# Performance work log

Hardware: AMD Instinct MI355X
Metric: run time of the kernel (lower is better)

## Reference

```python
import jax, jax.numpy as jnp
import numpy as np

K = 9          # kernel_size
PAD = K // 2   # 'same' padding, stride 1
SIGMA = 1.0
EPS = 1e-5     # BatchNorm eps

def _windows(a):
    # a: (B, C, L) -> (B, C, K, L); zero-padded sliding windows (== F.unfold semantics)
    L = a.shape[-1]
    ap = jnp.pad(a, ((0, 0), (0, 0), (PAD, PAD)))
    return jnp.stack([ap[:, :, k:k + L] for k in range(K)], axis=2)

def setup_inputs() -> dict:
    key = jax.random.key(0)
    ks = jax.random.split(key, 4)
    B, Cin, Cout, L = 8, 256, 256, 16384
    x = jax.random.normal(ks[0], (B, Cin, L), jnp.float32)
    coords = jax.random.uniform(ks[1], (B, 3, L), jnp.float32)
    conv_w = jax.random.normal(ks[2], (Cout, Cin, K), jnp.float32) * np.float32(1.0 / np.sqrt(Cin * K))
    conv_b = jnp.zeros((Cout,), jnp.float32)
    gamma = jnp.ones((Cout,), jnp.float32)
    beta = jnp.zeros((Cout,), jnp.float32)
    return {"x": x, "coords": coords, "conv_w": conv_w, "conv_b": conv_b, "gamma": gamma, "beta": beta}

def reference(x, coords, conv_w, conv_b, gamma, beta):
    # --- WeightedConv1D: Gaussian coordinate weights on each unfolded window element ---
    cw = _windows(coords)                                      # (B, 3, K, L)
    d2 = jnp.sum((cw - coords[:, :, None, :]) ** 2, axis=1)    # (B, K, L) squared dist to window center
    w = jnp.exp(-d2 / (2.0 * SIGMA ** 2))                      # (B, K, L) Gaussian weights
    xw = _windows(x) * w[:, None, :, :]                        # (B, Cin, K, L) weighted windows
    y = jnp.einsum('bckl,ock->bol', xw, conv_w) + conv_b[None, :, None]  # (B, Cout, L)
    # --- BatchNorm1d (training-mode batch statistics, biased variance) + ReLU ---
    mu = jnp.mean(y, axis=(0, 2), keepdims=True)
    var = jnp.var(y, axis=(0, 2), keepdims=True)
    yhat = (y - mu) * jax.lax.rsqrt(var + EPS)
    out = jax.nn.relu(yhat * gamma[None, :, None] + beta[None, :, None])
    # Dropout with drop=0.0 is the identity.
    return out
```

## Files before the change

### kernel.cpp

```cpp
#include <hip/hip_runtime.h>
#include <hip/hip_bf16.h>


typedef float        f32x4  __attribute__((ext_vector_type(4)));
typedef short        bf16x8 __attribute__((ext_vector_type(8)));
typedef unsigned int u32x4  __attribute__((ext_vector_type(4)));

#define LLEN 16384

__device__ __forceinline__ unsigned short bf16bits(float a) {
  return __builtin_bit_cast(unsigned short, __float2bfloat16(a));
}
__device__ __forceinline__ unsigned cvt_pk_bf16(float lo, float hi) {
  unsigned r;
  asm("v_cvt_pk_bf16_f32 %0, %1, %2" : "=v"(r) : "v"(lo), "v"(hi));
  return r;
}
__device__ __forceinline__ void gload16(const void* g, void* l) {
  __builtin_amdgcn_global_load_lds(
      (const __attribute__((address_space(1))) unsigned int*)g,
      (__attribute__((address_space(3))) unsigned int*)l, 16, 0, 0);
}
__device__ __forceinline__ float bflo(unsigned u) {
  return __builtin_bit_cast(float, u << 16);
}
__device__ __forceinline__ float bfhi(unsigned u) {
  return __builtin_bit_cast(float, u & 0xffff0000u);
}

__global__ void k_prep(const float* __restrict__ cw,
                       unsigned short* __restrict__ AU,
                       float* __restrict__ sums, int big) {
  const int idx = blockIdx.x * 256 + threadIdx.x;
  if (idx < 1024) sums[idx] = 0.0f;
  const int o   = idx / 2304;
  const int rem = idx - o * 2304;
  const int c   = rem / 9;
  const int kk  = rem - c * 9;
  const unsigned short bits = bf16bits(cw[idx]);
  if (big) {
    const int cc = c >> 6, c6 = c & 63;
    const int u = (c6 >> 3) ^ (o & 7);
    AU[(size_t)((kk * 4 + cc) << 14) + ((o * 8 + u) << 3) + (c6 & 7)] = bits;
  } else {
    AU[((size_t)kk * 256 + o) * 256 + c] = bits;
  }
}

__global__ void k_w(const float* __restrict__ coords, float* __restrict__ wbuf) {
  const int gidx = blockIdx.x * 256 + threadIdx.x;
  const int b = gidx >> 14, l = gidx & (LLEN - 1);
  const float* cb = coords + (size_t)b * 3 * LLEN;
  const float c0 = cb[l], c1 = cb[LLEN + l], c2v = cb[2 * LLEN + l];
#pragma unroll
  for (int kk = 0; kk < 9; ++kk) {
    const int lc = l + kk - 4;
    float a0 = 0.f, a1 = 0.f, a2 = 0.f;
    if (lc >= 0 && lc < LLEN) { a0 = cb[lc]; a1 = cb[LLEN + lc]; a2 = cb[2 * LLEN + lc]; }
    const float d0 = a0 - c0, d1 = a1 - c1, d2 = a2 - c2v;
    wbuf[(((size_t)(b * 9 + kk)) << 14) + l] = __expf(-0.5f * (d0 * d0 + d1 * d1 + d2 * d2));
  }
}

__global__ void k_xT(const float* __restrict__ x, unsigned short* __restrict__ xT) {
  __shared__ unsigned short T[64][72];
  const int tid = threadIdx.x, bid = blockIdx.x;
  const int ct = bid & 3, lt = (bid >> 2) & 255, b = bid >> 10;
  const int l0 = lt << 6, c0 = ct << 6;
#pragma unroll
  for (int p = 0; p < 4; ++p) {
    const int cl = p * 16 + (tid >> 4), ll = (tid & 15) << 2;
    const f32x4 v = *reinterpret_cast<const f32x4*>(
        x + (((size_t)(b * 256 + c0 + cl)) << 14) + l0 + ll);
#pragma unroll
    for (int q = 0; q < 4; ++q) T[cl][ll + q] = bf16bits(v[q]);
  }
  __syncthreads();
#pragma unroll
  for (int pass = 0; pass < 2; ++pass) {
    const int n = tid + pass * 256;
    const int ll = n >> 3, u = n & 7;
    const int l = l0 + ll;
    const int gsl = (u ^ (l & 7)) << 3;
    u32x4 val;
#pragma unroll
    for (int q = 0; q < 4; ++q)
      val[q] = (unsigned)T[gsl + 2 * q][ll] | ((unsigned)T[gsl + 2 * q + 1][ll] << 16);
    *reinterpret_cast<u32x4*>(xT + (((size_t)((b << 14) + l)) << 8) + (ct << 6) + (u << 3)) = val;
  }
}

template <int YBF>
__global__ __launch_bounds__(512, 2) void k_gemm16(
    const unsigned short* __restrict__ xT, const float* __restrict__ wbuf,
    const unsigned short* __restrict__ Agl, const float* __restrict__ convb,
    const unsigned short* __restrict__ zeros, float* __restrict__ yf,
    unsigned short* __restrict__ ybf, float* __restrict__ sums) {
  __shared__ __align__(16) unsigned short Ash[2][16384];
  __shared__ __align__(16) unsigned short Xsh[2][17408];

  const int tid = threadIdx.x, lane = tid & 63, wv = tid >> 6;
  const int wm = wv >> 2, wn = wv & 3;
  const int hi = lane >> 4, lo16 = lane & 15;
  const int b = blockIdx.x >> 6, lt = blockIdx.x & 63, l0 = lt << 8;
  const int nbase = wn * 64 + lo16;

  f32x4 acc[8][4];
#pragma unroll
  for (int i = 0; i < 8; ++i)
#pragma unroll
    for (int j = 0; j < 4; ++j) acc[i][j] = f32x4{0.f, 0.f, 0.f, 0.f};

  auto dmaA = [&](int ab, int kk, int cc) {
#pragma unroll
    for (int call = 0; call < 4; ++call) {
      const int n0 = ((call << 3) + wv) << 6;
      gload16(Agl + (((size_t)((kk << 2) + cc)) << 14) + (((size_t)(n0 + lane)) << 3),
              (char*)&Ash[ab][0] + n0 * 16);
    }
  };
  auto dmaX = [&](int xb, int ncc, int slot) {
    const int id = (slot << 3) + wv;
    if (id < 34) {
      const int n0 = id << 6;
      const int n = n0 + lane;
      const int r = n >> 3, u = n & 7;
      const int lp = l0 - 4 + r;
      const unsigned short* src =
          (lp >= 0 && lp < LLEN)
              ? xT + (((size_t)((b << 14) + lp)) << 8) + (ncc << 6) + (u << 3)
              : zeros;
      gload16(src, (char*)&Xsh[xb][0] + n0 * 16);
    }
  };

  dmaA(0, 0, 0);
#pragma unroll
  for (int s = 0; s < 5; ++s) dmaX(0, 0, s);
  float wl[4], wt[4];
#pragma unroll
  for (int nt = 0; nt < 4; ++nt)
    wl[nt] = wbuf[((size_t)(b * 9) << 14) + l0 + nbase + nt * 16];
  __syncthreads();

  int ab = 0;
#pragma unroll 1
  for (int cc = 0; cc < 4; ++cc) {
    const int xb = cc & 1;
    const char* XshB = (const char*)&Xsh[xb][0];
#pragma unroll 1
    for (int kk = 0; kk < 9; ++kk) {
      const bool last = (cc == 3) && (kk == 8);
      const int nkk = (kk == 8) ? 0 : kk + 1;
      const int ncc = (kk == 8) ? cc + 1 : cc;
      if (!last) {
        dmaA(ab ^ 1, nkk, ncc);
#pragma unroll
        for (int nt = 0; nt < 4; ++nt)
          wt[nt] = wbuf[((size_t)(b * 9 + nkk) << 14) + l0 + nbase + nt * 16];
      }
      if (cc < 3 && kk < 5) dmaX(xb ^ 1, cc + 1, kk);

      const char* AshB = (const char*)&Ash[ab][0];
      u32x4 xv0[4];
#pragma unroll
      for (int nt = 0; nt < 4; ++nt) {
        const int rr = nbase + nt * 16 + kk;
        xv0[nt] = *reinterpret_cast<const u32x4*>(
            XshB + rr * 128 + ((hi ^ ((rr + 4) & 7)) << 4));
      }
      bf16x8 a0[8];
#pragma unroll
      for (int mt = 0; mt < 8; ++mt) {
        const int o = wm * 128 + mt * 16 + lo16;
        a0[mt] = *reinterpret_cast<const bf16x8*>(
            AshB + o * 128 + ((hi ^ (lo16 & 7)) << 4));
      }
      bf16x8 b0[4];
#pragma unroll
      for (int nt = 0; nt < 4; ++nt) {
        u32x4 o4;
#pragma unroll
        for (int q = 0; q < 4; ++q)
          o4[q] = cvt_pk_bf16(bflo(xv0[nt][q]) * wl[nt], bfhi(xv0[nt][q]) * wl[nt]);
        b0[nt] = __builtin_bit_cast(bf16x8, o4);
      }
      u32x4 xv1[4];
#pragma unroll
      for (int nt = 0; nt < 4; ++nt) {
        const int rr = nbase + nt * 16 + kk;
        xv1[nt] = *reinterpret_cast<const u32x4*>(
            XshB + rr * 128 + (((4 + hi) ^ ((rr + 4) & 7)) << 4));
      }
#pragma unroll
      for (int mt = 0; mt < 8; ++mt)
#pragma unroll
        for (int nt = 0; nt < 4; ++nt)
          acc[mt][nt] = __builtin_amdgcn_mfma_f32_16x16x32_bf16(a0[mt], b0[nt],
                                                                acc[mt][nt], 0, 0, 0);
      bf16x8 a1[8];
#pragma unroll
      for (int mt = 0; mt < 8; ++mt) {
        const int o = wm * 128 + mt * 16 + lo16;
        a1[mt] = *reinterpret_cast<const bf16x8*>(
            AshB + o * 128 + (((4 + hi) ^ (lo16 & 7)) << 4));
      }
      bf16x8 b1[4];
#pragma unroll
      for (int nt = 0; nt < 4; ++nt) {
        u32x4 o4;
#pragma unroll
        for (int q = 0; q < 4; ++q)
          o4[q] = cvt_pk_bf16(bflo(xv1[nt][q]) * wl[nt], bfhi(xv1[nt][q]) * wl[nt]);
        b1[nt] = __builtin_bit_cast(bf16x8, o4);
      }
#pragma unroll
      for (int mt = 0; mt < 8; ++mt)
#pragma unroll
        for (int nt = 0; nt < 4; ++nt)
          acc[mt][nt] = __builtin_amdgcn_mfma_f32_16x16x32_bf16(a1[mt], b1[nt],
                                                                acc[mt][nt], 0, 0, 0);

      __syncthreads();
      ab ^= 1;
#pragma unroll
      for (int nt = 0; nt < 4; ++nt) wl[nt] = wt[nt];
    }
  }

  float* red = reinterpret_cast<float*>(&Xsh[0][0]);
  red[tid] = 0.0f;
  __syncthreads();
#pragma unroll
  for (int mt = 0; mt < 8; ++mt) {
#pragma unroll
    for (int v = 0; v < 4; ++v) {
      const int o = wm * 128 + mt * 16 + hi * 4 + v;
      const float cb = convb[o];
      float s = 0.f, s2 = 0.f;
#pragma unroll
      for (int nt = 0; nt < 4; ++nt) {
        const int l = l0 + nbase + nt * 16;
        const float yv = acc[mt][nt][v] + cb;
        const size_t idx = (((size_t)b * 256 + o) << 14) + l;
        if (YBF) ybf[idx] = bf16bits(yv);
        else     yf[idx] = yv;
        s += yv; s2 += yv * yv;
      }
#pragma unroll
      for (int d = 1; d < 16; d <<= 1) { s += __shfl_xor(s, d); s2 += __shfl_xor(s2, d); }
      if (lo16 == 0) { atomicAdd(&red[o], s); atomicAdd(&red[o + 256], s2); }
    }
  }
  __syncthreads();
  atomicAdd(&sums[tid], red[tid]);
}

__global__ __launch_bounds__(512, 2) void k_gemm_fb(
    const float* __restrict__ x, const float* __restrict__ wbuf,
    const unsigned short* __restrict__ Aperm, const float* __restrict__ convb,
    float* __restrict__ y, float* __restrict__ sums) {
  __shared__ __align__(16) unsigned short Ash[2][256 * 64];
  __shared__ __align__(16) unsigned short Xsh[2][264 * 72];

  const int tid  = threadIdx.x;
  const int lane = tid & 63, wv = tid >> 6;
  const int wm = wv >> 2, wn = wv & 3;
  const int hi = lane >> 4, lo16 = lane & 15;
  const int b  = blockIdx.x >> 6, lt = blockIdx.x & 63;
  const int l0 = lt << 8;
  const int nbase = wn * 64 + lo16;
  const int c = tid >> 3, rg = tid & 7;

  f32x4 acc[8][4];
#pragma unroll
  for (int i = 0; i < 8; ++i)
#pragma unroll
    for (int j = 0; j < 4; ++j) acc[i][j] = f32x4{0.f, 0.f, 0.f, 0.f};

  auto loadA = [&](int kk, int cc, u32x4 (&dst)[4]) {
#pragma unroll
    for (int p = 0; p < 4; ++p) {
      const int row = p * 64 + (tid >> 3);
      dst[p] = *reinterpret_cast<const u32x4*>(
          Aperm + ((size_t)kk * 256 + row) * 256 + cc * 64 + ((tid & 7) << 3));
    }
  };
  auto writeA = [&](int ab, const u32x4 (&src)[4]) {
#pragma unroll
    for (int p = 0; p < 4; ++p) {
      const int row  = p * 64 + (tid >> 3);
      const unsigned byte = (unsigned)(row * 128 + (((tid & 7) ^ (row & 7)) << 4));
      *reinterpret_cast<u32x4*>(reinterpret_cast<char*>(&Ash[ab][0]) + byte) = src[p];
    }
  };
  auto loadPiece = [&](int ncc, int i) -> f32x4 {
    const float* xrow = x + ((size_t)(b * 256 + ncc * 64 + c)) * LLEN;
    const int grp = rg + 8 * i;
    const int lx = l0 - 4 + grp * 4;
    f32x4 v = {0.f, 0.f, 0.f, 0.f};
    if (grp < 66 && lx >= 0 && lx <= LLEN - 4)
      v = *reinterpret_cast<const f32x4*>(xrow + lx);
    return v;
  };
  auto writePiece = [&](int xb, int i, const f32x4& v) {
    const int grp = rg + 8 * i;
    if (grp < 66) {
      unsigned short* base = &Xsh[xb][0] + (grp * 4) * 72 + c;
      base[0]   = bf16bits(v[0]);
      base[72]  = bf16bits(v[1]);
      base[144] = bf16bits(v[2]);
      base[216] = bf16bits(v[3]);
    }
  };

  {
    u32x4 a0[4];
    loadA(0, 0, a0);
    writeA(0, a0);
#pragma unroll
    for (int i = 0; i < 9; ++i) writePiece(0, i, loadPiece(0, i));
  }
  float wl[4];
#pragma unroll
  for (int nt = 0; nt < 4; ++nt)
    wl[nt] = wbuf[((size_t)(b * 9) << 14) + l0 + nbase + nt * 16];
  __syncthreads();

  int ab = 0;
  f32x4 xhold = {0.f, 0.f, 0.f, 0.f};

#pragma unroll 1
  for (int cc = 0; cc < 4; ++cc) {
    const int xb = cc & 1;
#pragma unroll 1
    for (int kk = 0; kk < 9; ++kk) {
      const int nkk = (kk == 8) ? 0 : kk + 1;
      const int ncc = (kk == 8) ? cc + 1 : cc;
      const bool has_next = (ncc < 4);

      u32x4 areg[4];
      if (has_next) loadA(nkk, ncc, areg);
      float wln[4] = {0.f, 0.f, 0.f, 0.f};
      if (has_next) {
#pragma unroll
        for (int nt = 0; nt < 4; ++nt)
          wln[nt] = wbuf[((size_t)(b * 9 + nkk) << 14) + l0 + nbase + nt * 16];
      }
      f32x4 xnew = {0.f, 0.f, 0.f, 0.f};
      if (cc < 3) xnew = loadPiece(cc + 1, kk);

      const char* AshB = reinterpret_cast<const char*>(&Ash[ab][0]);
      const char* XshB = reinterpret_cast<const char*>(&Xsh[xb][0]);
#pragma unroll
      for (int kb = 0; kb < 2; ++kb) {
        bf16x8 bfr[4];
#pragma unroll
        for (int nt = 0; nt < 4; ++nt) {
          const int r = nbase + nt * 16 + kk;
          const u32x4 xv = *reinterpret_cast<const u32x4*>(XshB + r * 144 + kb * 64 + hi * 16);
          u32x4 o4;
#pragma unroll
          for (int q = 0; q < 4; ++q)
            o4[q] = cvt_pk_bf16(bflo(xv[q]) * wl[nt], bfhi(xv[q]) * wl[nt]);
          bfr[nt] = __builtin_bit_cast(bf16x8, o4);
        }
#pragma unroll
        for (int mt = 0; mt < 8; ++mt) {
          const int orow = wm * 128 + mt * 16 + lo16;
          const unsigned aoff = (unsigned)(orow * 128 + (((kb * 4 + hi) ^ (orow & 7)) << 4));
          const bf16x8 af = *reinterpret_cast<const bf16x8*>(AshB + aoff);
#pragma unroll
          for (int nt = 0; nt < 4; ++nt)
            acc[mt][nt] = __builtin_amdgcn_mfma_f32_16x16x32_bf16(af, bfr[nt],
                                                                  acc[mt][nt], 0, 0, 0);
        }
      }

      if (cc < 3 && kk >= 1) writePiece(xb ^ 1, kk - 1, xhold);
      if (cc < 3 && kk == 8) writePiece(xb ^ 1, 8, xnew);
      if (has_next) writeA(ab ^ 1, areg);

      __syncthreads();
      ab ^= 1;
      xhold = xnew;
#pragma unroll
      for (int nt = 0; nt < 4; ++nt) wl[nt] = wln[nt];
    }
  }

  float* red = reinterpret_cast<float*>(&Ash[0][0]);
  red[tid] = 0.0f;
  __syncthreads();
#pragma unroll
  for (int mt = 0; mt < 8; ++mt) {
#pragma unroll
    for (int v = 0; v < 4; ++v) {
      const int o = wm * 128 + mt * 16 + hi * 4 + v;
      const float cb = convb[o];
      float s = 0.f, s2 = 0.f;
#pragma unroll
      for (int nt = 0; nt < 4; ++nt) {
        const int l = l0 + nbase + nt * 16;
        const float yv = acc[mt][nt][v] + cb;
        y[(((size_t)b * 256 + o) << 14) + l] = yv;
        s += yv; s2 += yv * yv;
      }
#pragma unroll
      for (int d = 1; d < 16; d <<= 1) { s += __shfl_xor(s, d); s2 += __shfl_xor(s2, d); }
      if (lo16 == 0) { atomicAdd(&red[o], s); atomicAdd(&red[o + 256], s2); }
    }
  }
  __syncthreads();
  atomicAdd(&sums[tid], red[tid]);
}

template <int YBF>
__global__ void k_norm(const float* __restrict__ yf, const unsigned short* __restrict__ ybf,
                       float* __restrict__ out, const float* __restrict__ sums,
                       const float* __restrict__ gamma, const float* __restrict__ beta) {
  const size_t i0 = ((size_t)blockIdx.x * 256 + threadIdx.x) * 8;
  const int o = (int)((i0 >> 14) & 255);
  const float n = 131072.f;
  const float mu = sums[o] / n;
  float var = sums[256 + o] / n - mu * mu;
  var = fmaxf(var, 0.f);
  const float sc = rsqrtf(var + 1e-5f) * gamma[o];
  const float bb = beta[o] - mu * sc;
  f32x4 v0, v1;
  if (YBF) {
    const u32x4 u = *reinterpret_cast<const u32x4*>(ybf + i0);
#pragma unroll
    for (int i = 0; i < 4; ++i) {
      const unsigned w = u[i];
      float a = bflo(w), c = bfhi(w);
      if (i < 2) { v0[2 * i] = a; v0[2 * i + 1] = c; }
      else       { v1[2 * (i - 2)] = a; v1[2 * (i - 2) + 1] = c; }
    }
  } else {
    v0 = *reinterpret_cast<const f32x4*>(yf + i0);
    v1 = *reinterpret_cast<const f32x4*>(yf + i0 + 4);
  }
#pragma unroll
  for (int i = 0; i < 4; ++i) {
    v0[i] = fmaxf(v0[i] * sc + bb, 0.f);
    v1[i] = fmaxf(v1[i] * sc + bb, 0.f);
  }
  *reinterpret_cast<f32x4*>(out + i0) = v0;
  *reinterpret_cast<f32x4*>(out + i0 + 4) = v1;
}

extern "C" void kernel_launch(void* const* d_in, const int* in_sizes, int n_in,
                              void* d_out, int out_size, void* d_ws, size_t ws_size,
                              hipStream_t stream) {
  const float* x      = (const float*)d_in[0];
  const float* coords = (const float*)d_in[1];
  const float* conv_w = (const float*)d_in[2];
  const float* conv_b = (const float*)d_in[3];
  const float* gamma  = (const float*)d_in[4];
  const float* beta   = (const float*)d_in[5];
  float* out = (float*)d_out;

  float* sums = (float*)d_ws;
  const unsigned short* zeros = (const unsigned short*)((char*)d_ws + 2048);
  float* wbuf = (float*)((char*)d_ws + 4096);
  unsigned short* AU  = (unsigned short*)((char*)d_ws + 4096 + (size_t)8 * 9 * LLEN * 4);
  unsigned short* xT  = AU + 589824;
  unsigned short* ybf = xT + 33554432;
  const size_t need_big = 4096 + (size_t)8 * 9 * LLEN * 4 + 1179648ull + 67108864ull;
  const size_t need_ybf = need_big + 67108864ull;
  const int big  = (ws_size >= need_big) ? 1 : 0;
  const int ybfp = (ws_size >= need_ybf) ? 1 : 0;

  k_prep<<<2304, 256, 0, stream>>>(conv_w, AU, sums, big);
  k_w<<<512, 256, 0, stream>>>(coords, wbuf);
  if (big) {
    k_xT<<<8192, 256, 0, stream>>>(x, xT);
    if (ybfp) {
      k_gemm16<1><<<512, 512, 0, stream>>>(xT, wbuf, AU, conv_b, zeros, out, ybf, sums);
      k_norm<1><<<16384, 256, 0, stream>>>(out, ybf, out, sums, gamma, beta);
    } else {
      k_gemm16<0><<<512, 512, 0, stream>>>(xT, wbuf, AU, conv_b, zeros, out, ybf, sums);
      k_norm<0><<<16384, 256, 0, stream>>>(out, ybf, out, sums, gamma, beta);
    }
  } else {
    k_gemm_fb<<<512, 512, 0, stream>>>(x, wbuf, AU, conv_b, out, sums);
    k_norm<0><<<16384, 256, 0, stream>>>(out, (const unsigned short*)out, out, sums, gamma, beta);
  }
}
```

Before: 254.4 us.

## Pre-weight X tile into LDS per tap instead of scaling in MFMA loop

The GEMM kernel now loads raw bf16 x rows into registers, multiplies them by the Gaussian weight for the next tap, and writes the weighted bf16 tile into a double-buffered LDS buffer after each MFMA step. The inner loop then reads ready-to-use B fragments with no per-fragment unpack, multiply and convert. The intent is to take VALU conversion work off the MFMA critical path and reuse each weighted element across the wave's N tiles. The cost is an extra LDS store pass and a register-staged x prefetch per tap, in place of the async global-to-LDS DMA, so VALU and LDS traffic move into a separate staging phase.

```diff
diff --git a/kernel.cpp b/kernel.cpp
--- a/kernel.cpp
+++ b/kernel.cpp
@@ -91,19 +91,20 @@
 }
 
 template <int YBF>
-__global__ __launch_bounds__(512, 2) void k_gemm16(
+__global__ __launch_bounds__(512, 2) void k_gemm16w(
     const unsigned short* __restrict__ xT, const float* __restrict__ wbuf,
     const unsigned short* __restrict__ Agl, const float* __restrict__ convb,
-    const unsigned short* __restrict__ zeros, float* __restrict__ yf,
-    unsigned short* __restrict__ ybf, float* __restrict__ sums) {
+    float* __restrict__ yf, unsigned short* __restrict__ ybf,
+    float* __restrict__ sums) {
   __shared__ __align__(16) unsigned short Ash[2][16384];
-  __shared__ __align__(16) unsigned short Xsh[2][17408];
+  __shared__ __align__(16) unsigned short Xw[2][264 * 64];
 
   const int tid = threadIdx.x, lane = tid & 63, wv = tid >> 6;
   const int wm = wv >> 2, wn = wv & 3;
   const int hi = lane >> 4, lo16 = lane & 15;
   const int b = blockIdx.x >> 6, lt = blockIdx.x & 63, l0 = lt << 8;
   const int nbase = wn * 64 + lo16;
+  const int rbase = tid >> 3, uu = tid & 7;
 
   f32x4 acc[8][4];
 #pragma unroll
@@ -119,55 +120,79 @@
               (char*)&Ash[ab][0] + n0 * 16);
     }
   };
-  auto dmaX = [&](int xb, int ncc, int slot) {
-    const int id = (slot << 3) + wv;
-    if (id < 34) {
-      const int n0 = id << 6;
-      const int n = n0 + lane;
-      const int r = n >> 3, u = n & 7;
-      const int lp = l0 - 4 + r;
-      const unsigned short* src =
-          (lp >= 0 && lp < LLEN)
-              ? xT + (((size_t)((b << 14) + lp)) << 8) + (ncc << 6) + (u << 3)
-              : zeros;
-      gload16(src, (char*)&Xsh[xb][0] + n0 * 16);
-    }
-  };
-
+  auto loadX = [&](int cc, int i) -> u32x4 {
+    u32x4 v = {0u, 0u, 0u, 0u};
+    if (i < 4 || tid < 64) {
+      const int r = rbase + 64 * i;
+      const int l = l0 - 4 + r;
+      if (l >= 0 && l < LLEN)
+        v = *reinterpret_cast<const u32x4*>(
+            xT + (((size_t)((b << 14) + l)) << 8) + cc * 64 + uu * 8);
+    }
+    return v;
+  };
+  auto loadW = [&](int nkk, float (&ws5)[5]) {
+    const float* wrow = wbuf + ((size_t)(b * 9 + nkk) << 14);
+#pragma unroll
+    for (int i = 0; i < 5; ++i) {
+      if (i < 4 || tid < 64) {
+        const int r = rbase + 64 * i;
+        int li = l0 + r - nkk;
+        li = li < 0 ? 0 : (li > LLEN - 1 ? LLEN - 1 : li);
+        ws5[i] = wrow[li];
+      }
+    }
+  };
+  auto stage = [&](int xwb, const u32x4 (&xr)[5], const float (&ws5)[5]) {
+#pragma unroll
+    for (int i = 0; i < 5; ++i) {
+      if (i < 4 || tid < 64) {
+        const int r = rbase + 64 * i;
+        const float wv2 = ws5[i];
+        u32x4 o4;
+#pragma unroll
+        for (int q = 0; q < 4; ++q)
+          o4[q] = cvt_pk_bf16(bflo(xr[i][q]) * wv2, bfhi(xr[i][q]) * wv2);
+        *reinterpret_cast<u32x4*>(
+            reinterpret_cast<char*>(&Xw[xwb][0]) + r * 128 + (uu << 4)) = o4;
+      }
+    }
+  };
+
+  u32x4 xcur[5], xnext[5];
+#pragma unroll
+  for (int i = 0; i < 5; ++i) xcur[i] = loadX(0, i);
   dmaA(0, 0, 0);
-#pragma unroll
-  for (int s = 0; s < 5; ++s) dmaX(0, 0, s);
-  float wl[4], wt[4];
-#pragma unroll
-  for (int nt = 0; nt < 4; ++nt)
-    wl[nt] = wbuf[((size_t)(b * 9) << 14) + l0 + nbase + nt * 16];
-  __syncthreads();
-
-  int ab = 0;
+  {
+    float ws5[5];
+    loadW(0, ws5);
+    stage(0, xcur, ws5);
+  }
+  __syncthreads();
+
+  int ab = 0, xwb = 0;
 #pragma unroll 1
   for (int cc = 0; cc < 4; ++cc) {
-    const int xb = cc & 1;
-    const char* XshB = (const char*)&Xsh[xb][0];
 #pragma unroll 1
     for (int kk = 0; kk < 9; ++kk) {
       const bool last = (cc == 3) && (kk == 8);
       const int nkk = (kk == 8) ? 0 : kk + 1;
       const int ncc = (kk == 8) ? cc + 1 : cc;
-      if (!last) {
-        dmaA(ab ^ 1, nkk, ncc);
-#pragma unroll
-        for (int nt = 0; nt < 4; ++nt)
-          wt[nt] = wbuf[((size_t)(b * 9 + nkk) << 14) + l0 + nbase + nt * 16];
-      }
-      if (cc < 3 && kk < 5) dmaX(xb ^ 1, cc + 1, kk);
+
+      float ws5[5];
+      if (!last) loadW(nkk, ws5);
+      if (!last) dmaA(ab ^ 1, nkk, ncc);
+      if (cc < 3 && kk >= 4) xnext[kk - 4] = loadX(cc + 1, kk - 4);
 
       const char* AshB = (const char*)&Ash[ab][0];
-      u32x4 xv0[4];
+      const char* XwB  = (const char*)&Xw[xwb][0];
+      bf16x8 b0[4], b1[4];
 #pragma unroll
       for (int nt = 0; nt < 4; ++nt) {
         const int rr = nbase + nt * 16 + kk;
-        xv0[nt] = *reinterpret_cast<const u32x4*>(
-            XshB + rr * 128 + ((hi ^ ((rr + 4) & 7)) << 4));
+        const int sw = (rr + 4) & 7;
+        b0[nt] = *reinterpret_cast<const bf16x8*>(XwB + rr * 128 + ((hi ^ sw) << 4));
+        b1[nt] = *reinterpret_cast<const bf16x8*>(XwB + rr * 128 + (((4 + hi) ^ sw) << 4));
       }
       bf16x8 a0[8];
 #pragma unroll
@@ -176,22 +201,6 @@
         a0[mt] = *reinterpret_cast<const bf16x8*>(
             AshB + o * 128 + ((hi ^ (lo16 & 7)) << 4));
       }
-      bf16x8 b0[4];
-#pragma unroll
-      for (int nt = 0; nt < 4; ++nt) {
-        u32x4 o4;
-#pragma unroll
-        for (int q = 0; q < 4; ++q)
-          o4[q] = cvt_pk_bf16(bflo(xv0[nt][q]) * wl[nt], bfhi(xv0[nt][q]) * wl[nt]);
-        b0[nt] = __builtin_bit_cast(bf16x8, o4);
-      }
-      u32x4 xv1[4];
-#pragma unroll
-      for (int nt = 0; nt < 4; ++nt) {
-        const int rr = nbase + nt * 16 + kk;
-        xv1[nt] = *reinterpret_cast<const u32x4*>(
-            XshB + rr * 128 + (((4 + hi) ^ ((rr + 4) & 7)) << 4));
-      }
 #pragma unroll
       for (int mt = 0; mt < 8; ++mt)
 #pragma unroll
@@ -205,15 +214,6 @@
         a1[mt] = *reinterpret_cast<const bf16x8*>(
             AshB + o * 128 + (((4 + hi) ^ (lo16 & 7)) << 4));
       }
-      bf16x8 b1[4];
-#pragma unroll
-      for (int nt = 0; nt < 4; ++nt) {
-        u32x4 o4;
-#pragma unroll
-        for (int q = 0; q < 4; ++q)
-          o4[q] = cvt_pk_bf16(bflo(xv1[nt][q]) * wl[nt], bfhi(xv1[nt][q]) * wl[nt]);
-        b1[nt] = __builtin_bit_cast(bf16x8, o4);
-      }
 #pragma unroll
       for (int mt = 0; mt < 8; ++mt)
 #pragma unroll
@@ -221,14 +221,20 @@
           acc[mt][nt] = __builtin_amdgcn_mfma_f32_16x16x32_bf16(a1[mt], b1[nt],
                                                                 acc[mt][nt], 0, 0, 0);
 
+      if (!last) {
+        if (kk < 8) stage(xwb ^ 1, xcur, ws5);
+        else        stage(xwb ^ 1, xnext, ws5);
+      }
       __syncthreads();
-      ab ^= 1;
-#pragma unroll
-      for (int nt = 0; nt < 4; ++nt) wl[nt] = wt[nt];
-    }
-  }
-
-  float* red = reinterpret_cast<float*>(&Xsh[0][0]);
+      ab ^= 1; xwb ^= 1;
+    }
+    if (cc < 3) {
+#pragma unroll
+      for (int i = 0; i < 5; ++i) xcur[i] = xnext[i];
+    }
+  }
+
+  float* red = reinterpret_cast<float*>(&Xw[0][0]);
   red[tid] = 0.0f;
   __syncthreads();
 #pragma unroll
@@ -462,7 +468,6 @@
   float* out = (float*)d_out;
 
   float* sums = (float*)d_ws;
-  const unsigned short* zeros = (const unsigned short*)((char*)d_ws + 2048);
   float* wbuf = (float*)((char*)d_ws + 4096);
   unsigned short* AU  = (unsigned short*)((char*)d_ws + 4096 + (size_t)8 * 9 * LLEN * 4);
   unsigned short* xT  = AU + 589824;
@@ -477,10 +482,10 @@
   if (big) {
     k_xT<<<8192, 256, 0, stream>>>(x, xT);
     if (ybfp) {
-      k_gemm16<1><<<512, 512, 0, stream>>>(xT, wbuf, AU, conv_b, zeros, out, ybf, sums);
+      k_gemm16w<1><<<512, 512, 0, stream>>>(xT, wbuf, AU, conv_b, out, ybf, sums);
       k_norm<1><<<16384, 256, 0, stream>>>(out, ybf, out, sums, gamma, beta);
     } else {
-      k_gemm16<0><<<512, 512, 0, stream>>>(xT, wbuf, AU, conv_b, zeros, out, ybf, sums);
+      k_gemm16w<0><<<512, 512, 0, stream>>>(xT, wbuf, AU, conv_b, out, ybf, sums);
       k_norm<0><<<16384, 256, 0, stream>>>(out, ybf, out, sums, gamma, beta);
     }
   } else {
```

After: 285.7 us. +12.3%, slower.

## Load GEMM B operand directly from global memory instead of LDS staging

Applied to the files above, without the earlier changes.

The GEMM kernel stops staging the transposed x tile (with halo) into double-buffered shared memory through async LDS DMA. Each thread now reads its B-operand fragments straight from global memory every kk step, with bounds checks replacing the zero buffer. This frees about 68KB of LDS and its DMA scheduling, which may help occupancy. In exchange it adds latency-exposed global loads in the inner loop and re-reads overlapping window rows from cache nine times.

```diff
diff --git a/kernel.cpp b/kernel.cpp
--- a/kernel.cpp
+++ b/kernel.cpp
@@ -91,13 +91,12 @@
 }
 
 template <int YBF>
-__global__ __launch_bounds__(512, 2) void k_gemm16(
+__global__ __launch_bounds__(512, 2) void k_gemm16g(
     const unsigned short* __restrict__ xT, const float* __restrict__ wbuf,
     const unsigned short* __restrict__ Agl, const float* __restrict__ convb,
-    const unsigned short* __restrict__ zeros, float* __restrict__ yf,
-    unsigned short* __restrict__ ybf, float* __restrict__ sums) {
+    float* __restrict__ yf, unsigned short* __restrict__ ybf,
+    float* __restrict__ sums) {
   __shared__ __align__(16) unsigned short Ash[2][16384];
-  __shared__ __align__(16) unsigned short Xsh[2][17408];
 
   const int tid = threadIdx.x, lane = tid & 63, wv = tid >> 6;
   const int wm = wv >> 2, wn = wv & 3;
@@ -119,24 +118,25 @@
               (char*)&Ash[ab][0] + n0 * 16);
     }
   };
-  auto dmaX = [&](int xb, int ncc, int slot) {
-    const int id = (slot << 3) + wv;
-    if (id < 34) {
-      const int n0 = id << 6;
-      const int n = n0 + lane;
-      const int r = n >> 3, u = n & 7;
-      const int lp = l0 - 4 + r;
-      const unsigned short* src =
-          (lp >= 0 && lp < LLEN)
-              ? xT + (((size_t)((b << 14) + lp)) << 8) + (ncc << 6) + (u << 3)
-              : zeros;
-      gload16(src, (char*)&Xsh[xb][0] + n0 * 16);
+  auto loadB = [&](int kk, int cc, u32x4 (&v0)[4], u32x4 (&v1)[4]) {
+#pragma unroll
+    for (int nt = 0; nt < 4; ++nt) {
+      const int lg = l0 + nbase + nt * 16 + kk - 4;
+      const bool ok = (lg >= 0) && (lg < LLEN);
+      const int lc = ok ? lg : 0;
+      const unsigned short* rowp =
+          xT + (((size_t)((b << 14) + lc)) << 8) + cc * 64;
+      const int sw = lc & 7;
+      u32x4 t0 = {0u, 0u, 0u, 0u}, t1 = {0u, 0u, 0u, 0u};
+      if (ok) {
+        t0 = *reinterpret_cast<const u32x4*>(rowp + ((hi ^ sw) << 3));
+        t1 = *reinterpret_cast<const u32x4*>(rowp + (((4 + hi) ^ sw) << 3));
+      }
+      v0[nt] = t0; v1[nt] = t1;
     }
   };
 
   dmaA(0, 0, 0);
-#pragma unroll
-  for (int s = 0; s < 5; ++s) dmaX(0, 0, s);
   float wl[4], wt[4];
 #pragma unroll
   for (int nt = 0; nt < 4; ++nt)
@@ -146,29 +146,22 @@
   int ab = 0;
 #pragma unroll 1
   for (int cc = 0; cc < 4; ++cc) {
-    const int xb = cc & 1;
-    const char* XshB = (const char*)&Xsh[xb][0];
 #pragma unroll 1
     for (int kk = 0; kk < 9; ++kk) {
       const bool last = (cc == 3) && (kk == 8);
       const int nkk = (kk == 8) ? 0 : kk + 1;
       const int ncc = (kk == 8) ? cc + 1 : cc;
+
+      u32x4 xv0[4], xv1[4];
+      loadB(kk, cc, xv0, xv1);
       if (!last) {
-        dmaA(ab ^ 1, nkk, ncc);
 #pragma unroll
         for (int nt = 0; nt < 4; ++nt)
           wt[nt] = wbuf[((size_t)(b * 9 + nkk) << 14) + l0 + nbase + nt * 16];
-      }
-      if (cc < 3 && kk < 5) dmaX(xb ^ 1, cc + 1, kk);
+        dmaA(ab ^ 1, nkk, ncc);
+      }
 
       const char* AshB = (const char*)&Ash[ab][0];
-      u32x4 xv0[4];
-#pragma unroll
-      for (int nt = 0; nt < 4; ++nt) {
-        const int rr = nbase + nt * 16 + kk;
-        xv0[nt] = *reinterpret_cast<const u32x4*>(
-            XshB + rr * 128 + ((hi ^ ((rr + 4) & 7)) << 4));
-      }
       bf16x8 a0[8];
 #pragma unroll
       for (int mt = 0; mt < 8; ++mt) {
@@ -185,13 +178,6 @@
           o4[q] = cvt_pk_bf16(bflo(xv0[nt][q]) * wl[nt], bfhi(xv0[nt][q]) * wl[nt]);
         b0[nt] = __builtin_bit_cast(bf16x8, o4);
       }
-      u32x4 xv1[4];
-#pragma unroll
-      for (int nt = 0; nt < 4; ++nt) {
-        const int rr = nbase + nt * 16 + kk;
-        xv1[nt] = *reinterpret_cast<const u32x4*>(
-            XshB + rr * 128 + (((4 + hi) ^ ((rr + 4) & 7)) << 4));
-      }
 #pragma unroll
       for (int mt = 0; mt < 8; ++mt)
 #pragma unroll
@@ -228,7 +214,7 @@
     }
   }
 
-  float* red = reinterpret_cast<float*>(&Xsh[0][0]);
+  __shared__ float red[512];
   red[tid] = 0.0f;
   __syncthreads();
 #pragma unroll
@@ -462,7 +448,6 @@
   float* out = (float*)d_out;
 
   float* sums = (float*)d_ws;
-  const unsigned short* zeros = (const unsigned short*)((char*)d_ws + 2048);
   float* wbuf = (float*)((char*)d_ws + 4096);
   unsigned short* AU  = (unsigned short*)((char*)d_ws + 4096 + (size_t)8 * 9 * LLEN * 4);
   unsigned short* xT  = AU + 589824;
@@ -477,10 +462,10 @@
   if (big) {
     k_xT<<<8192, 256, 0, stream>>>(x, xT);
     if (ybfp) {
-      k_gemm16<1><<<512, 512, 0, stream>>>(xT, wbuf, AU, conv_b, zeros, out, ybf, sums);
+      k_gemm16g<1><<<512, 512, 0, stream>>>(xT, wbuf, AU, conv_b, out, ybf, sums);
       k_norm<1><<<16384, 256, 0, stream>>>(out, ybf, out, sums, gamma, beta);
     } else {
-      k_gemm16<0><<<512, 512, 0, stream>>>(xT, wbuf, AU, conv_b, zeros, out, ybf, sums);
+      k_gemm16g<0><<<512, 512, 0, stream>>>(xT, wbuf, AU, conv_b, out, ybf, sums);
       k_norm<0><<<16384, 256, 0, stream>>>(out, ybf, out, sums, gamma, beta);
     }
   } else {
```

After: 309.4 us. +21.6%, slower.
